# Kernel tuning notes

Hardware: AMD Instinct MI355X
Metric: run time of the kernel (lower is better)

Reference implementation:

```python
import jax, jax.numpy as jnp
import numpy as np

B, Fc, C, H, D, L = 128, 256, 256, 8, 32, 6  # batch, columns, dim, heads, head_dim, layers


def _ln(x, g, b, eps=1e-5):
    m = x.mean(-1, keepdims=True)
    v = ((x - m) ** 2).mean(-1, keepdims=True)
    return (x - m) * jax.lax.rsqrt(v + eps) * g + b


def setup_inputs() -> dict:
    key = jax.random.key(0)
    ks = jax.random.split(key, 16)
    s = 0.02  # weight init scale to keep 6-layer activations stable
    return {
        "x": jax.random.normal(ks[0], (B, Fc, C), jnp.float32),
        "col_emb": jax.random.normal(ks[1], (1, Fc, C), jnp.float32),
        "pos_emb": jax.random.normal(ks[2], (1, Fc + 1, C), jnp.float32),
        "col_bias": jax.random.normal(ks[3], (Fc, Fc), jnp.float32),
        "ln1_g": jnp.ones((L, C), jnp.float32),
        "ln1_b": jnp.zeros((L, C), jnp.float32),
        "qkv_w": jax.random.normal(ks[4], (L, C, 3 * C), jnp.float32) * s,
        "qkv_b": jnp.zeros((L, 3 * C), jnp.float32),
        "out_w": jax.random.normal(ks[5], (L, C, C), jnp.float32) * s,
        "out_b": jnp.zeros((L, C), jnp.float32),
        "ln2_g": jnp.ones((L, C), jnp.float32),
        "ln2_b": jnp.zeros((L, C), jnp.float32),
        "w1": jax.random.normal(ks[6], (L, C, 4 * C), jnp.float32) * s,
        "b1": jnp.zeros((L, 4 * C), jnp.float32),
        "w2": jax.random.normal(ks[7], (L, 4 * C, 2 * C), jnp.float32) * s,
        "b2": jnp.zeros((L, 2 * C), jnp.float32),
        "w3": jax.random.normal(ks[8], (L, C, C), jnp.float32) * s,
        "b3": jnp.zeros((L, C), jnp.float32),
        "fin_g": jnp.ones((C,), jnp.float32),
        "fin_b": jnp.zeros((C,), jnp.float32),
    }


def reference(x, col_emb, pos_emb, col_bias, ln1_g, ln1_b, qkv_w, qkv_b,
              out_w, out_b, ln2_g, ln2_b, w1, b1, w2, b2, w3, b3, fin_g, fin_b):
    Fdim = x.shape[1]
    h = x + col_emb[:, :Fdim] + pos_emb[:, 1:Fdim + 1]
    bias = col_bias[:Fdim, :Fdim]  # [T, T]
    scale = 1.0 / np.sqrt(D).astype(np.float32)
    params = (ln1_g, ln1_b, qkv_w, qkv_b, out_w, out_b, ln2_g, ln2_b,
              w1, b1, w2, b2, w3, b3)

    def block(xc, p):
        g1, be1, qw, qb, ow, ob, g2, be2, W1, B1, W2, B2, W3, B3 = p
        Bn, T, Cd = xc.shape
        hn = _ln(xc, g1, be1)
        qkv = hn @ qw + qb                              # [B,T,3C]
        q, k, v = jnp.split(qkv, 3, axis=-1)
        q = q.reshape(Bn, T, H, D)
        k = k.reshape(Bn, T, H, D)
        v = v.reshape(Bn, T, H, D)
        scores = jnp.einsum('bthd,bshd->bhts', q, k) * scale + bias[None, None]
        w = jax.nn.softmax(scores, axis=-1)             # dropout = identity (eval)
        attn = jnp.einsum('bhts,bshd->bthd', w, v).reshape(Bn, T, Cd)
        attn = attn @ ow + ob
        attn = attn + bias[None]                        # [1,T,T] broadcast, T==C
        xc = xc + attn
        hn2 = _ln(xc, g2, be2)
        u = jax.nn.gelu(hn2 @ W1 + B1, approximate=False)
        gl = u @ W2 + B2                                # [B,T,2C]
        a, gate = jnp.split(gl, 2, axis=-1)
        xc = xc + (a * jax.nn.sigmoid(gate)) @ W3 + B3
        return xc, None

    h, _ = jax.lax.scan(block, h, params)
    h = _ln(h, fin_g, fin_b)
    return h.mean(axis=1)  # pooling='mean' -> [B, C]
```

## Files before the change

kernel.cpp:

```cpp
#include <hip/hip_runtime.h>

typedef __bf16 bx8 __attribute__((ext_vector_type(8)));
typedef float fx4 __attribute__((ext_vector_type(4)));

#define GAS(p) ((const __attribute__((address_space(1))) void*)(const void*)(p))
#define LAS(p) ((__attribute__((address_space(3))) void*)(void*)(p))
#define WAITVM(n) do { asm volatile("s_waitcnt vmcnt(" #n ")" ::: "memory"); \
                       __builtin_amdgcn_sched_barrier(0); } while (0)
#define WAITLG0() do { asm volatile("s_waitcnt lgkmcnt(0)" ::: "memory"); \
                       __builtin_amdgcn_sched_barrier(0); } while (0)

__device__ __forceinline__ unsigned short f2bf(float f) {
  return __builtin_bit_cast(unsigned short, (__bf16)f);
}
__device__ __forceinline__ float bf2f(unsigned short s) {
  unsigned u = ((unsigned)s) << 16;
  return __builtin_bit_cast(float, u);
}

__global__ __launch_bounds__(256) void wtrans_kernel(const float* __restrict__ src,
                                                     unsigned short* __restrict__ dst,
                                                     int K, int N) {
  __shared__ unsigned short t[64][68];
  const int l = blockIdx.z;
  const float* s = src + (size_t)l * K * N;
  unsigned short* d = dst + (size_t)l * N * K;
  const int n0 = blockIdx.x * 64, k0 = blockIdx.y * 64;
  const int tx = threadIdx.x & 63, ty = threadIdx.x >> 6;
#pragma unroll
  for (int r = 0; r < 64; r += 4)
    t[tx][ty + r] = f2bf(s[(size_t)(k0 + ty + r) * N + n0 + tx]);
  __syncthreads();
#pragma unroll
  for (int r = 0; r < 64; r += 4)
    d[(size_t)(n0 + ty + r) * K + k0 + tx] = t[ty + r][tx];
}

__global__ __launch_bounds__(256) void embed_kernel(const float4* __restrict__ x,
                                                    const float4* __restrict__ ce,
                                                    const float4* __restrict__ pe,
                                                    float4* __restrict__ o) {
  int i = blockIdx.x * 256 + threadIdx.x;
  int c4 = i & 63;
  int t = (i >> 6) & 255;
  float4 a = x[i], b = ce[t * 64 + c4], p = pe[(t + 1) * 64 + c4];
  o[i] = make_float4(a.x + b.x + p.x, a.y + b.y + p.y, a.z + b.z + p.z, a.w + b.w + p.w);
}

template <int MODE>
__global__ __launch_bounds__(256) void ln_kernel(const float* __restrict__ x,
                                                 const float* __restrict__ gw,
                                                 const float* __restrict__ bw,
                                                 unsigned short* __restrict__ out,
                                                 float2* __restrict__ stats) {
  int row = blockIdx.x * 4 + (threadIdx.x >> 6);
  int lane = threadIdx.x & 63;
  const float4 v = *(const float4*)(x + (size_t)row * 256 + lane * 4);
  float s = v.x + v.y + v.z + v.w;
  float q = v.x * v.x + v.y * v.y + v.z * v.z + v.w * v.w;
#pragma unroll
  for (int off = 1; off < 64; off <<= 1) {
    s += __shfl_xor(s, off);
    q += __shfl_xor(q, off);
  }
  float mean = s * (1.0f / 256.0f);
  float rs = rsqrtf(q * (1.0f / 256.0f) - mean * mean + 1e-5f);
  if (MODE == 1) {
    if (lane == 0) stats[row] = make_float2(mean, rs);
    return;
  }
  float4 gv = *(const float4*)(gw + lane * 4);
  float4 bv = *(const float4*)(bw + lane * 4);
  ushort4 o;
  o.x = f2bf((v.x - mean) * rs * gv.x + bv.x);
  o.y = f2bf((v.y - mean) * rs * gv.y + bv.y);
  o.z = f2bf((v.z - mean) * rs * gv.z + bv.z);
  o.w = f2bf((v.w - mean) * rs * gv.w + bv.w);
  *(ushort4*)(out + (size_t)row * 256 + lane * 4) = o;
}

__global__ __launch_bounds__(256) void mean_part_kernel(const float* __restrict__ x,
                                                        const float2* __restrict__ stats,
                                                        float* __restrict__ part) {
  int b = blockIdx.x, half = blockIdx.y, c = threadIdx.x;
  const float* xb = x + (size_t)b * 65536 + half * 32768;
  const float2* st = stats + b * 256 + half * 128;
  float acc = 0.f;
#pragma unroll 4
  for (int t = 0; t < 128; ++t) {
    float2 s = st[t];
    acc += (xb[t * 256 + c] - s.x) * s.y;
  }
  part[(size_t)(b * 2 + half) * 256 + c] = acc;
}
__global__ __launch_bounds__(256) void mean_fin_kernel(const float* __restrict__ part,
                                                       const float* __restrict__ fg,
                                                       const float* __restrict__ fb,
                                                       float* __restrict__ out) {
  int b = blockIdx.x, c = threadIdx.x;
  out[b * 256 + c] =
      (part[(size_t)(2 * b) * 256 + c] + part[(size_t)(2 * b + 1) * 256 + c]) *
          (1.0f / 256.0f) * fg[c] + fb[c];
}

template <int EP>
__global__ __launch_bounds__(256) void gemm_kernel(const unsigned short* __restrict__ A,
                                                   const unsigned short* __restrict__ BT,
                                                   const float* __restrict__ bvec,
                                                   const float* __restrict__ cbias,
                                                   float* __restrict__ resid,
                                                   unsigned short* __restrict__ outb,
                                                   int N, int K) {
  __shared__ unsigned short lA[2][128 * 32];
  __shared__ unsigned short lB[2][128 * 32];
  const int tid = threadIdx.x;
  const int lane = tid & 63, w = tid >> 6;
  const int wr = w >> 1, wc = w & 1;
  const int g = lane >> 4, lr = lane & 15;
  const int m0 = blockIdx.y * 128, n0 = blockIdx.x * 128;
  fx4 acc[4][4] = {};

  auto STAGE = [&](int buf, int kk) {
#pragma unroll
    for (int r = 0; r < 2; ++r) {
      int u = r * 256 + tid;
      int row = u >> 2, sl = u & 3;
      int c = sl ^ ((row >> 1) & 3);
      __builtin_amdgcn_global_load_lds(GAS(A + (size_t)(m0 + row) * K + kk + c * 8),
                                       LAS(&lA[buf][u * 8]), 16, 0, 0);
      __builtin_amdgcn_global_load_lds(GAS(BT + (size_t)(n0 + row) * K + kk + c * 8),
                                       LAS(&lB[buf][u * 8]), 16, 0, 0);
    }
  };

  const int nt = K >> 5;
  STAGE(0, 0);
  STAGE(1, 32);
  for (int t = 0; t < nt; ++t) {
    if (t == nt - 1) WAITVM(0); else WAITVM(4);
    __builtin_amdgcn_s_barrier();
    const int buf = t & 1;
    bx8 af[4], bq[4];
#pragma unroll
    for (int i = 0; i < 4; ++i) {
      int row = wr * 64 + i * 16 + lr;
      af[i] = *(const bx8*)&lA[buf][row * 32 + (g ^ ((row >> 1) & 3)) * 8];
      int col = wc * 64 + i * 16 + lr;
      bq[i] = *(const bx8*)&lB[buf][col * 32 + (g ^ ((col >> 1) & 3)) * 8];
    }
    WAITLG0();
    __builtin_amdgcn_s_barrier();
    if (t + 2 < nt) STAGE(buf, (t + 2) * 32);
#pragma unroll
    for (int i = 0; i < 4; ++i)
#pragma unroll
      for (int j = 0; j < 4; ++j)
        acc[i][j] = __builtin_amdgcn_mfma_f32_16x16x32_bf16(bq[j], af[i], acc[i][j], 0, 0, 0);
  }

#pragma unroll
  for (int i = 0; i < 4; ++i) {
    const int m = m0 + wr * 64 + i * 16 + lr;
#pragma unroll
    for (int j = 0; j < 4; ++j) {
      const int nc = n0 + wc * 64 + j * 16 + g * 4;
      const float4 bv = *(const float4*)(bvec + nc);
      float v0 = acc[i][j][0] + bv.x, v1 = acc[i][j][1] + bv.y;
      float v2 = acc[i][j][2] + bv.z, v3 = acc[i][j][3] + bv.w;
      if constexpr (EP == 1) {
        v0 = 0.5f * v0 * (1.0f + erff(v0 * 0.70710678118654752f));
        v1 = 0.5f * v1 * (1.0f + erff(v1 * 0.70710678118654752f));
        v2 = 0.5f * v2 * (1.0f + erff(v2 * 0.70710678118654752f));
        v3 = 0.5f * v3 * (1.0f + erff(v3 * 0.70710678118654752f));
      }
      if constexpr (EP == 0 || EP == 1) {
        ushort4 st;
        st.x = f2bf(v0); st.y = f2bf(v1); st.z = f2bf(v2); st.w = f2bf(v3);
        *(ushort4*)(outb + (size_t)m * N + nc) = st;
      } else {
        if (nc < 512) {
          ushort4 st;
          st.x = f2bf(v0); st.y = f2bf(v1); st.z = f2bf(v2); st.w = f2bf(v3);
          *(ushort4*)(outb + (size_t)m * N + nc) = st;
        } else {
          unsigned short* vTp = (unsigned short*)resid;
          const int s = m & 255, b = m >> 8;
          const int hv = nc - 512;
          const int h = hv >> 5, d0 = hv & 31;
          const int jj = (s & 3) + 4 * ((s >> 4) & 1);
          const int ub = (s >> 5) * 128 + ((s >> 2) & 3) * 32 + d0;
          unsigned short* base = vTp + (size_t)(b * 8 + h) * 8192;
          const float vv[4] = {v0, v1, v2, v3};
#pragma unroll
          for (int r = 0; r < 4; ++r) {
            int u = ub + r;
            int up = (u & ~7) | ((u & 7) ^ ((u >> 3) & 7));
            base[up * 8 + jj] = f2bf(vv[r]);
          }
        }
      }
    }
  }
}

template <int EP>
__global__ __launch_bounds__(256) void gemm64_kernel(const unsigned short* __restrict__ A,
                                                     const unsigned short* __restrict__ BT,
                                                     const float* __restrict__ bvec,
                                                     const float* __restrict__ cbias,
                                                     float* __restrict__ resid,
                                                     int N, int K) {
  __shared__ unsigned short lA[2][64 * 32];
  __shared__ unsigned short lB[2][128 * 32];
  const int tid = threadIdx.x;
  const int lane = tid & 63, w = tid >> 6;
  const int g = lane >> 4, lr = lane & 15;
  const int m0 = blockIdx.y * 64, n0 = blockIdx.x * 128;
  fx4 acc[4][2] = {};

  auto STAGE = [&](int buf, int kk) {
    {
      int u = tid;
      int row = u >> 2, sl = u & 3;
      int c = sl ^ ((row >> 1) & 3);
      __builtin_amdgcn_global_load_lds(GAS(A + (size_t)(m0 + row) * K + kk + c * 8),
                                       LAS(&lA[buf][u * 8]), 16, 0, 0);
    }
#pragma unroll
    for (int r = 0; r < 2; ++r) {
      int u = r * 256 + tid;
      int row = u >> 2, sl = u & 3;
      int c = sl ^ ((row >> 1) & 3);
      __builtin_amdgcn_global_load_lds(GAS(BT + (size_t)(n0 + row) * K + kk + c * 8),
                                       LAS(&lB[buf][u * 8]), 16, 0, 0);
    }
  };

  const int nt = K >> 5;
  STAGE(0, 0);
  STAGE(1, 32);
  for (int t = 0; t < nt; ++t) {
    if (t == nt - 1) WAITVM(0); else WAITVM(3);
    __builtin_amdgcn_s_barrier();
    const int buf = t & 1;
    bx8 af[4], bq[2];
#pragma unroll
    for (int i = 0; i < 4; ++i) {
      int row = i * 16 + lr;
      af[i] = *(const bx8*)&lA[buf][row * 32 + (g ^ ((row >> 1) & 3)) * 8];
    }
#pragma unroll
    for (int j = 0; j < 2; ++j) {
      int col = w * 32 + j * 16 + lr;
      bq[j] = *(const bx8*)&lB[buf][col * 32 + (g ^ ((col >> 1) & 3)) * 8];
    }
    WAITLG0();
    __builtin_amdgcn_s_barrier();
    if (t + 2 < nt) STAGE(buf, (t + 2) * 32);
#pragma unroll
    for (int i = 0; i < 4; ++i)
#pragma unroll
      for (int j = 0; j < 2; ++j)
        acc[i][j] = __builtin_amdgcn_mfma_f32_16x16x32_bf16(bq[j], af[i], acc[i][j], 0, 0, 0);
  }

#pragma unroll
  for (int i = 0; i < 4; ++i) {
    const int m = m0 + i * 16 + lr;
#pragma unroll
    for (int j = 0; j < 2; ++j) {
      const int nc = n0 + w * 32 + j * 16 + g * 4;
      const float4 bv = *(const float4*)(bvec + nc);
      float v0 = acc[i][j][0] + bv.x, v1 = acc[i][j][1] + bv.y;
      float v2 = acc[i][j][2] + bv.z, v3 = acc[i][j][3] + bv.w;
      if constexpr (EP == 2) {
        const float4 cb = *(const float4*)(cbias + (size_t)(m & 255) * 256 + nc);
        v0 += cb.x; v1 += cb.y; v2 += cb.z; v3 += cb.w;
      }
      float4* rp = (float4*)(resid + (size_t)m * N + nc);
      float4 old = *rp;
      *rp = make_float4(old.x + v0, old.y + v1, old.z + v2, old.w + v3);
    }
  }
}

__global__ __launch_bounds__(256) void gemm_w2f64_kernel(const unsigned short* __restrict__ A,
                                                         const unsigned short* __restrict__ BT,
                                                         const float* __restrict__ b2,
                                                         unsigned short* __restrict__ gout) {
  __shared__ unsigned short lA[2][64 * 32];
  __shared__ unsigned short lBa[2][128 * 32];
  __shared__ unsigned short lBg[2][128 * 32];
  const int tid = threadIdx.x;
  const int lane = tid & 63, w = tid >> 6;
  const int g = lane >> 4, lr = lane & 15;
  const int m0 = blockIdx.y * 64, n0 = blockIdx.x * 128;
  fx4 aA[4][2] = {}, aG[4][2] = {};

  auto STAGE = [&](int buf, int kk) {
    {
      int u = tid;
      int row = u >> 2, sl = u & 3;
      int c = sl ^ ((row >> 1) & 3);
      __builtin_amdgcn_global_load_lds(GAS(A + (size_t)(m0 + row) * 1024 + kk + c * 8),
                                       LAS(&lA[buf][u * 8]), 16, 0, 0);
    }
#pragma unroll
    for (int r = 0; r < 2; ++r) {
      int u = r * 256 + tid;
      int row = u >> 2, sl = u & 3;
      int c = sl ^ ((row >> 1) & 3);
      __builtin_amdgcn_global_load_lds(GAS(BT + (size_t)(n0 + row) * 1024 + kk + c * 8),
                                       LAS(&lBa[buf][u * 8]), 16, 0, 0);
      __builtin_amdgcn_global_load_lds(GAS(BT + (size_t)(256 + n0 + row) * 1024 + kk + c * 8),
                                       LAS(&lBg[buf][u * 8]), 16, 0, 0);
    }
  };

  STAGE(0, 0);
  STAGE(1, 32);
  for (int t = 0; t < 32; ++t) {
    if (t == 31) WAITVM(0); else WAITVM(5);
    __builtin_amdgcn_s_barrier();
    const int buf = t & 1;
    bx8 af[4], ba[2], bg[2];
#pragma unroll
    for (int i = 0; i < 4; ++i) {
      int row = i * 16 + lr;
      af[i] = *(const bx8*)&lA[buf][row * 32 + (g ^ ((row >> 1) & 3)) * 8];
    }
#pragma unroll
    for (int j = 0; j < 2; ++j) {
      int col = w * 32 + j * 16 + lr;
      int sw = (g ^ ((col >> 1) & 3)) * 8;
      ba[j] = *(const bx8*)&lBa[buf][col * 32 + sw];
      bg[j] = *(const bx8*)&lBg[buf][col * 32 + sw];
    }
    WAITLG0();
    __builtin_amdgcn_s_barrier();
    if (t + 2 < 32) STAGE(buf, (t + 2) * 32);
#pragma unroll
    for (int i = 0; i < 4; ++i)
#pragma unroll
      for (int j = 0; j < 2; ++j) {
        aA[i][j] = __builtin_amdgcn_mfma_f32_16x16x32_bf16(ba[j], af[i], aA[i][j], 0, 0, 0);
        aG[i][j] = __builtin_amdgcn_mfma_f32_16x16x32_bf16(bg[j], af[i], aG[i][j], 0, 0, 0);
      }
  }

#pragma unroll
  for (int i = 0; i < 4; ++i) {
    const int m = m0 + i * 16 + lr;
#pragma unroll
    for (int j = 0; j < 2; ++j) {
      const int nc = n0 + w * 32 + j * 16 + g * 4;
      const float4 bva = *(const float4*)(b2 + nc);
      const float4 bvg = *(const float4*)(b2 + 256 + nc);
      float a0 = aA[i][j][0] + bva.x, a1 = aA[i][j][1] + bva.y;
      float a2 = aA[i][j][2] + bva.z, a3 = aA[i][j][3] + bva.w;
      float g0 = aG[i][j][0] + bvg.x, g1 = aG[i][j][1] + bvg.y;
      float g2 = aG[i][j][2] + bvg.z, g3 = aG[i][j][3] + bvg.w;
      ushort4 st;
      st.x = f2bf(a0 / (1.0f + __expf(-g0)));
      st.y = f2bf(a1 / (1.0f + __expf(-g1)));
      st.z = f2bf(a2 / (1.0f + __expf(-g2)));
      st.w = f2bf(a3 / (1.0f + __expf(-g3)));
      *(ushort4*)(gout + (size_t)m * 256 + nc) = st;
    }
  }
}

__global__ __launch_bounds__(256) void attn_kernel(const unsigned short* __restrict__ qkv,
                                                   const unsigned short* __restrict__ vT,
                                                   const float* __restrict__ cbias,
                                                   unsigned short* __restrict__ attnb) {
  __shared__ unsigned short Kl[256 * 32];
  __shared__ unsigned short Vl[1024 * 8];
  const int bh = blockIdx.x, b = bh >> 3, h = bh & 7;
  const int tid = threadIdx.x, lane = tid & 63, w = tid >> 6;
  const int g = lane >> 4, lr = lane & 15;
  const unsigned short* qb_ = qkv + (size_t)b * 196608;
  const unsigned short* vTb = vT + (size_t)bh * 8192;
#pragma unroll
  for (int r = 0; r < 4; ++r) {
    int u = r * 256 + tid;
    int s = u >> 2, sl = u & 3;
    int c = sl ^ ((s >> 1) & 3);
    __builtin_amdgcn_global_load_lds(GAS(qb_ + (size_t)s * 768 + 256 + h * 32 + c * 8),
                                     LAS(&Kl[u * 8]), 16, 0, 0);
    __builtin_amdgcn_global_load_lds(GAS(vTb + u * 8), LAS(&Vl[u * 8]), 16, 0, 0);
  }
  asm volatile("s_waitcnt vmcnt(0)" ::: "memory");
  __syncthreads();
  const float scale = 0.17677669529663689f;
  const fx4 zero = {0.f, 0.f, 0.f, 0.f};
#pragma unroll 1
  for (int it = 0; it < 4; ++it) {
    const int t = it * 64 + w * 16 + lr;
    bx8 qf = *(const bx8*)(qb_ + (size_t)t * 768 + h * 32 + g * 8);
    float p[16][4];
    float mx = -1e30f;
#pragma unroll
    for (int n = 0; n < 16; ++n) {
      int sr = n * 16 + lr;
      bx8 kf = *(const bx8*)&Kl[sr * 32 + (g ^ ((sr >> 1) & 3)) * 8];
      fx4 sc = __builtin_amdgcn_mfma_f32_16x16x32_bf16(kf, qf, zero, 0, 0, 0);
      const float4 cb = *(const float4*)(cbias + (size_t)t * 256 + n * 16 + g * 4);
      p[n][0] = sc[0] * scale + cb.x;
      p[n][1] = sc[1] * scale + cb.y;
      p[n][2] = sc[2] * scale + cb.z;
      p[n][3] = sc[3] * scale + cb.w;
      mx = fmaxf(mx, fmaxf(fmaxf(p[n][0], p[n][1]), fmaxf(p[n][2], p[n][3])));
    }
    mx = fmaxf(mx, __shfl_xor(mx, 16));
    mx = fmaxf(mx, __shfl_xor(mx, 32));
    float sum = 0.f;
    bx8 bq[8];
#pragma unroll
    for (int c = 0; c < 8; ++c) {
      union { bx8 v; unsigned short u[8]; } pk;
#pragma unroll
      for (int jj = 0; jj < 8; ++jj) {
        float e = __expf(p[2 * c + (jj >> 2)][jj & 3] - mx);
        sum += e;
        pk.u[jj] = f2bf(e);
      }
      bq[c] = pk.v;
    }
    sum += __shfl_xor(sum, 16);
    sum += __shfl_xor(sum, 32);
    const float inv = 1.0f / sum;
    fx4 oa0 = zero, oa1 = zero;
#pragma unroll
    for (int c = 0; c < 8; ++c) {
      int u0 = c * 128 + g * 32 + lr;
      int u0p = (u0 & ~7) | ((u0 & 7) ^ ((u0 >> 3) & 7));
      bx8 vf0 = *(const bx8*)&Vl[u0p * 8];
      oa0 = __builtin_amdgcn_mfma_f32_16x16x32_bf16(vf0, bq[c], oa0, 0, 0, 0);
      int u1 = u0 + 16;
      int u1p = (u1 & ~7) | ((u1 & 7) ^ ((u1 >> 3) & 7));
      bx8 vf1 = *(const bx8*)&Vl[u1p * 8];
      oa1 = __builtin_amdgcn_mfma_f32_16x16x32_bf16(vf1, bq[c], oa1, 0, 0, 0);
    }
    ushort4 o0, o1;
    o0.x = f2bf(oa0[0] * inv); o0.y = f2bf(oa0[1] * inv);
    o0.z = f2bf(oa0[2] * inv); o0.w = f2bf(oa0[3] * inv);
    o1.x = f2bf(oa1[0] * inv); o1.y = f2bf(oa1[1] * inv);
    o1.z = f2bf(oa1[2] * inv); o1.w = f2bf(oa1[3] * inv);
    unsigned short* orow = attnb + (size_t)(b * 256 + t) * 256 + h * 32;
    *(ushort4*)(orow + 4 * g) = o0;
    *(ushort4*)(orow + 16 + 4 * g) = o1;
  }
}

extern "C" void kernel_launch(void* const* d_in, const int* in_sizes, int n_in,
                              void* d_out, int out_size, void* d_ws, size_t ws_size,
                              hipStream_t stream) {
  (void)in_sizes; (void)n_in; (void)out_size; (void)ws_size;
  const float* x     = (const float*)d_in[0];
  const float* cemb  = (const float*)d_in[1];
  const float* pemb  = (const float*)d_in[2];
  const float* cbias = (const float*)d_in[3];
  const float* ln1g  = (const float*)d_in[4];
  const float* ln1b  = (const float*)d_in[5];
  const float* qkvw  = (const float*)d_in[6];
  const float* qkvb  = (const float*)d_in[7];
  const float* outw  = (const float*)d_in[8];
  const float* outbv = (const float*)d_in[9];
  const float* ln2g  = (const float*)d_in[10];
  const float* ln2b  = (const float*)d_in[11];
  const float* w1    = (const float*)d_in[12];
  const float* b1    = (const float*)d_in[13];
  const float* w2    = (const float*)d_in[14];
  const float* b2    = (const float*)d_in[15];
  const float* w3    = (const float*)d_in[16];
  const float* b3    = (const float*)d_in[17];
  const float* fing  = (const float*)d_in[18];
  const float* finb  = (const float*)d_in[19];

  char* ws = (char*)d_ws;
  float* x_res = (float*)(ws);
  unsigned short* hn   = (unsigned short*)(ws + 33554432);
  unsigned short* big  = (unsigned short*)(ws + 50331648);
  unsigned short* vT   = (unsigned short*)(ws + 100663296);
  unsigned short* wT   = (unsigned short*)(ws + 117440512);
  float2* stats = (float2*)(ws + 130809856);
  float* part  = (float*)big;

  unsigned short* qkvwT = wT;
  unsigned short* outwT = wT + 1179648;
  unsigned short* w1T   = wT + 1572864;
  unsigned short* w2T   = wT + 3145728;
  unsigned short* w3T   = wT + 6291456;

  wtrans_kernel<<<dim3(12, 4, 6), 256, 0, stream>>>(qkvw, qkvwT, 256, 768);
  wtrans_kernel<<<dim3(4, 4, 6), 256, 0, stream>>>(outw, outwT, 256, 256);
  wtrans_kernel<<<dim3(16, 4, 6), 256, 0, stream>>>(w1, w1T, 256, 1024);
  wtrans_kernel<<<dim3(8, 16, 6), 256, 0, stream>>>(w2, w2T, 1024, 512);
  wtrans_kernel<<<dim3(4, 4, 6), 256, 0, stream>>>(w3, w3T, 256, 256);
  embed_kernel<<<8192, 256, 0, stream>>>((const float4*)x, (const float4*)cemb,
                                         (const float4*)pemb, (float4*)x_res);
  for (int l = 0; l < 6; ++l) {
    ln_kernel<0><<<8192, 256, 0, stream>>>(x_res, ln1g + l * 256, ln1b + l * 256, hn, nullptr);
    gemm_kernel<4><<<dim3(6, 256), 256, 0, stream>>>(hn, qkvwT + (size_t)l * 196608,
                                                     qkvb + l * 768, nullptr, (float*)vT,
                                                     big, 768, 256);
    attn_kernel<<<1024, 256, 0, stream>>>(big, vT, cbias, hn);
    gemm64_kernel<2><<<dim3(2, 512), 256, 0, stream>>>(hn, outwT + (size_t)l * 65536,
                                                       outbv + l * 256, cbias, x_res,
                                                       256, 256);
    ln_kernel<0><<<8192, 256, 0, stream>>>(x_res, ln2g + l * 256, ln2b + l * 256, hn, nullptr);
    gemm_kernel<1><<<dim3(8, 256), 256, 0, stream>>>(hn, w1T + (size_t)l * 262144,
                                                     b1 + l * 1024, nullptr, nullptr, big,
                                                     1024, 256);
    gemm_w2f64_kernel<<<dim3(2, 512), 256, 0, stream>>>(big, w2T + (size_t)l * 524288,
                                                        b2 + l * 512, hn);
    gemm64_kernel<3><<<dim3(2, 512), 256, 0, stream>>>(hn, w3T + (size_t)l * 65536,
                                                       b3 + l * 256, nullptr, x_res,
                                                       256, 256);
  }
  ln_kernel<1><<<8192, 256, 0, stream>>>(x_res, nullptr, nullptr, nullptr, stats);
  mean_part_kernel<<<dim3(128, 2), 256, 0, stream>>>(x_res, stats, part);
  mean_fin_kernel<<<128, 256, 0, stream>>>(part, fing, finb, (float*)d_out);
}
```

Measured before the change: 1.540 ms.

## Fuse LayerNorm into residual GEMM epilogues and embedding, widen GEMM tiles

Removes the standalone LayerNorm launches by computing row statistics inside the out-proj and W3 GEMM epilogues, which now cover full 256-wide rows per block, and by fusing the first LN into the embedding kernel. The final-layer W3 GEMM writes mean/rstd stats for pooling directly. The gated W2 GEMM moves to 128x128 tiles, and attention hoists its Q fragment loads ahead of the K/V wait. This cuts 13 full-tensor read/write passes and launches, at the cost of fewer blocks for the fused GEMMs (512) and more registers and LDS per block.

```diff
diff --git a/kernel.cpp b/kernel.cpp
--- a/kernel.cpp
+++ b/kernel.cpp
@@ -36,26 +36,20 @@
     d[(size_t)(n0 + ty + r) * K + k0 + tx] = t[ty + r][tx];
 }
 
-__global__ __launch_bounds__(256) void embed_kernel(const float4* __restrict__ x,
-                                                    const float4* __restrict__ ce,
-                                                    const float4* __restrict__ pe,
-                                                    float4* __restrict__ o) {
-  int i = blockIdx.x * 256 + threadIdx.x;
-  int c4 = i & 63;
-  int t = (i >> 6) & 255;
-  float4 a = x[i], b = ce[t * 64 + c4], p = pe[(t + 1) * 64 + c4];
-  o[i] = make_float4(a.x + b.x + p.x, a.y + b.y + p.y, a.z + b.z + p.z, a.w + b.w + p.w);
-}
-
-template <int MODE>
-__global__ __launch_bounds__(256) void ln_kernel(const float* __restrict__ x,
-                                                 const float* __restrict__ gw,
-                                                 const float* __restrict__ bw,
-                                                 unsigned short* __restrict__ out,
-                                                 float2* __restrict__ stats) {
-  int row = blockIdx.x * 4 + (threadIdx.x >> 6);
-  int lane = threadIdx.x & 63;
-  const float4 v = *(const float4*)(x + (size_t)row * 256 + lane * 4);
+__global__ __launch_bounds__(256) void embed_ln_kernel(const float4* __restrict__ x,
+                                                       const float4* __restrict__ ce,
+                                                       const float4* __restrict__ pe,
+                                                       const float* __restrict__ gw,
+                                                       const float* __restrict__ bw,
+                                                       float4* __restrict__ xres,
+                                                       unsigned short* __restrict__ hn) {
+  const int row = blockIdx.x * 4 + (threadIdx.x >> 6);
+  const int lane = threadIdx.x & 63;
+  const int t = row & 255;
+  const size_t idx = (size_t)row * 64 + lane;
+  float4 a = x[idx], b = ce[t * 64 + lane], p = pe[(t + 1) * 64 + lane];
+  float4 v = make_float4(a.x + b.x + p.x, a.y + b.y + p.y, a.z + b.z + p.z, a.w + b.w + p.w);
+  xres[idx] = v;
   float s = v.x + v.y + v.z + v.w;
   float q = v.x * v.x + v.y * v.y + v.z * v.z + v.w * v.w;
 #pragma unroll
@@ -65,10 +59,6 @@
   }
   float mean = s * (1.0f / 256.0f);
   float rs = rsqrtf(q * (1.0f / 256.0f) - mean * mean + 1e-5f);
-  if (MODE == 1) {
-    if (lane == 0) stats[row] = make_float2(mean, rs);
-    return;
-  }
   float4 gv = *(const float4*)(gw + lane * 4);
   float4 bv = *(const float4*)(bw + lane * 4);
   ushort4 o;
@@ -76,7 +66,7 @@
   o.y = f2bf((v.y - mean) * rs * gv.y + bv.y);
   o.z = f2bf((v.z - mean) * rs * gv.z + bv.z);
   o.w = f2bf((v.w - mean) * rs * gv.w + bv.w);
-  *(ushort4*)(out + (size_t)row * 256 + lane * 4) = o;
+  *(ushort4*)(hn + (size_t)row * 256 + lane * 4) = o;
 }
 
 __global__ __launch_bounds__(256) void mean_part_kernel(const float* __restrict__ x,
@@ -107,7 +97,6 @@
 __global__ __launch_bounds__(256) void gemm_kernel(const unsigned short* __restrict__ A,
                                                    const unsigned short* __restrict__ BT,
                                                    const float* __restrict__ bvec,
-                                                   const float* __restrict__ cbias,
                                                    float* __restrict__ resid,
                                                    unsigned short* __restrict__ outb,
                                                    int N, int K) {
@@ -173,7 +162,7 @@
         v2 = 0.5f * v2 * (1.0f + erff(v2 * 0.70710678118654752f));
         v3 = 0.5f * v3 * (1.0f + erff(v3 * 0.70710678118654752f));
       }
-      if constexpr (EP == 0 || EP == 1) {
+      if constexpr (EP == 1) {
         ushort4 st;
         st.x = f2bf(v0); st.y = f2bf(v1); st.z = f2bf(v2); st.w = f2bf(v3);
         *(ushort4*)(outb + (size_t)m * N + nc) = st;
@@ -203,20 +192,25 @@
   }
 }
 
-template <int EP>
-__global__ __launch_bounds__(256) void gemm64_kernel(const unsigned short* __restrict__ A,
-                                                     const unsigned short* __restrict__ BT,
-                                                     const float* __restrict__ bvec,
-                                                     const float* __restrict__ cbias,
-                                                     float* __restrict__ resid,
-                                                     int N, int K) {
+template <int EP, int LNM>
+__global__ __launch_bounds__(256) void gemm_ln_kernel(const unsigned short* __restrict__ A,
+                                                      const unsigned short* __restrict__ BT,
+                                                      const float* __restrict__ bvec,
+                                                      const float* __restrict__ cbias,
+                                                      float* __restrict__ resid,
+                                                      const float* __restrict__ lnw,
+                                                      const float* __restrict__ lnb,
+                                                      unsigned short* __restrict__ hn,
+                                                      float2* __restrict__ stats,
+                                                      int K) {
   __shared__ unsigned short lA[2][64 * 32];
-  __shared__ unsigned short lB[2][128 * 32];
+  __shared__ unsigned short lB[2][256 * 32];
+  __shared__ float2 red[4][64];
   const int tid = threadIdx.x;
   const int lane = tid & 63, w = tid >> 6;
   const int g = lane >> 4, lr = lane & 15;
-  const int m0 = blockIdx.y * 64, n0 = blockIdx.x * 128;
-  fx4 acc[4][2] = {};
+  const int m0 = blockIdx.x * 64;
+  fx4 acc[4][4] = {};
 
   auto STAGE = [&](int buf, int kk) {
     {
@@ -227,11 +221,11 @@
                                        LAS(&lA[buf][u * 8]), 16, 0, 0);
     }
 #pragma unroll
-    for (int r = 0; r < 2; ++r) {
+    for (int r = 0; r < 4; ++r) {
       int u = r * 256 + tid;
       int row = u >> 2, sl = u & 3;
       int c = sl ^ ((row >> 1) & 3);
-      __builtin_amdgcn_global_load_lds(GAS(BT + (size_t)(n0 + row) * K + kk + c * 8),
+      __builtin_amdgcn_global_load_lds(GAS(BT + (size_t)row * K + kk + c * 8),
                                        LAS(&lB[buf][u * 8]), 16, 0, 0);
     }
   };
@@ -240,18 +234,18 @@
   STAGE(0, 0);
   STAGE(1, 32);
   for (int t = 0; t < nt; ++t) {
-    if (t == nt - 1) WAITVM(0); else WAITVM(3);
+    if (t == nt - 1) WAITVM(0); else WAITVM(5);
     __builtin_amdgcn_s_barrier();
     const int buf = t & 1;
-    bx8 af[4], bq[2];
+    bx8 af[4], bq[4];
 #pragma unroll
     for (int i = 0; i < 4; ++i) {
       int row = i * 16 + lr;
       af[i] = *(const bx8*)&lA[buf][row * 32 + (g ^ ((row >> 1) & 3)) * 8];
     }
 #pragma unroll
-    for (int j = 0; j < 2; ++j) {
-      int col = w * 32 + j * 16 + lr;
+    for (int j = 0; j < 4; ++j) {
+      int col = w * 64 + j * 16 + lr;
       bq[j] = *(const bx8*)&lB[buf][col * 32 + (g ^ ((col >> 1) & 3)) * 8];
     }
     WAITLG0();
@@ -260,16 +254,17 @@
 #pragma unroll
     for (int i = 0; i < 4; ++i)
 #pragma unroll
-      for (int j = 0; j < 2; ++j)
+      for (int j = 0; j < 4; ++j)
         acc[i][j] = __builtin_amdgcn_mfma_f32_16x16x32_bf16(bq[j], af[i], acc[i][j], 0, 0, 0);
   }
 
+  float s[4] = {0.f, 0.f, 0.f, 0.f}, q[4] = {0.f, 0.f, 0.f, 0.f};
 #pragma unroll
   for (int i = 0; i < 4; ++i) {
     const int m = m0 + i * 16 + lr;
 #pragma unroll
-    for (int j = 0; j < 2; ++j) {
-      const int nc = n0 + w * 32 + j * 16 + g * 4;
+    for (int j = 0; j < 4; ++j) {
+      const int nc = w * 64 + j * 16 + g * 4;
       const float4 bv = *(const float4*)(bvec + nc);
       float v0 = acc[i][j][0] + bv.x, v1 = acc[i][j][1] + bv.y;
       float v2 = acc[i][j][2] + bv.z, v3 = acc[i][j][3] + bv.w;
@@ -277,39 +272,82 @@
         const float4 cb = *(const float4*)(cbias + (size_t)(m & 255) * 256 + nc);
         v0 += cb.x; v1 += cb.y; v2 += cb.z; v3 += cb.w;
       }
-      float4* rp = (float4*)(resid + (size_t)m * N + nc);
+      float4* rp = (float4*)(resid + (size_t)m * 256 + nc);
       float4 old = *rp;
-      *rp = make_float4(old.x + v0, old.y + v1, old.z + v2, old.w + v3);
-    }
-  }
-}
-
-__global__ __launch_bounds__(256) void gemm_w2f64_kernel(const unsigned short* __restrict__ A,
-                                                         const unsigned short* __restrict__ BT,
-                                                         const float* __restrict__ b2,
-                                                         unsigned short* __restrict__ gout) {
-  __shared__ unsigned short lA[2][64 * 32];
+      v0 += old.x; v1 += old.y; v2 += old.z; v3 += old.w;
+      *rp = make_float4(v0, v1, v2, v3);
+      acc[i][j][0] = v0; acc[i][j][1] = v1; acc[i][j][2] = v2; acc[i][j][3] = v3;
+      s[i] += v0 + v1 + v2 + v3;
+      q[i] += v0 * v0 + v1 * v1 + v2 * v2 + v3 * v3;
+    }
+  }
+#pragma unroll
+  for (int i = 0; i < 4; ++i) {
+    s[i] += __shfl_xor(s[i], 16); s[i] += __shfl_xor(s[i], 32);
+    q[i] += __shfl_xor(q[i], 16); q[i] += __shfl_xor(q[i], 32);
+  }
+  if (lane < 16) {
+#pragma unroll
+    for (int i = 0; i < 4; ++i) red[w][i * 16 + lr] = make_float2(s[i], q[i]);
+  }
+  __syncthreads();
+  float mean[4], rs[4];
+#pragma unroll
+  for (int i = 0; i < 4; ++i) {
+    float2 r0 = red[0][i * 16 + lr], r1 = red[1][i * 16 + lr];
+    float2 r2 = red[2][i * 16 + lr], r3 = red[3][i * 16 + lr];
+    float S = r0.x + r1.x + r2.x + r3.x;
+    float Q = r0.y + r1.y + r2.y + r3.y;
+    mean[i] = S * (1.0f / 256.0f);
+    rs[i] = rsqrtf(Q * (1.0f / 256.0f) - mean[i] * mean[i] + 1e-5f);
+  }
+  if constexpr (LNM == 1) {
+    if (w == 0 && g == 0) {
+#pragma unroll
+      for (int i = 0; i < 4; ++i) stats[m0 + i * 16 + lr] = make_float2(mean[i], rs[i]);
+    }
+  } else {
+#pragma unroll
+    for (int i = 0; i < 4; ++i) {
+      const int m = m0 + i * 16 + lr;
+#pragma unroll
+      for (int j = 0; j < 4; ++j) {
+        const int nc = w * 64 + j * 16 + g * 4;
+        const float4 gv = *(const float4*)(lnw + nc);
+        const float4 bv2 = *(const float4*)(lnb + nc);
+        ushort4 st;
+        st.x = f2bf((acc[i][j][0] - mean[i]) * rs[i] * gv.x + bv2.x);
+        st.y = f2bf((acc[i][j][1] - mean[i]) * rs[i] * gv.y + bv2.y);
+        st.z = f2bf((acc[i][j][2] - mean[i]) * rs[i] * gv.z + bv2.z);
+        st.w = f2bf((acc[i][j][3] - mean[i]) * rs[i] * gv.w + bv2.w);
+        *(ushort4*)(hn + (size_t)m * 256 + nc) = st;
+      }
+    }
+  }
+}
+
+__global__ __launch_bounds__(256) void gemm_w2f_kernel(const unsigned short* __restrict__ A,
+                                                       const unsigned short* __restrict__ BT,
+                                                       const float* __restrict__ b2,
+                                                       unsigned short* __restrict__ gout) {
+  __shared__ unsigned short lA[2][128 * 32];
   __shared__ unsigned short lBa[2][128 * 32];
   __shared__ unsigned short lBg[2][128 * 32];
   const int tid = threadIdx.x;
   const int lane = tid & 63, w = tid >> 6;
+  const int wr = w >> 1, wc = w & 1;
   const int g = lane >> 4, lr = lane & 15;
-  const int m0 = blockIdx.y * 64, n0 = blockIdx.x * 128;
-  fx4 aA[4][2] = {}, aG[4][2] = {};
+  const int m0 = blockIdx.y * 128, n0 = blockIdx.x * 128;
+  fx4 aA[4][4] = {}, aG[4][4] = {};
 
   auto STAGE = [&](int buf, int kk) {
-    {
-      int u = tid;
+#pragma unroll
+    for (int r = 0; r < 2; ++r) {
+      int u = r * 256 + tid;
       int row = u >> 2, sl = u & 3;
       int c = sl ^ ((row >> 1) & 3);
       __builtin_amdgcn_global_load_lds(GAS(A + (size_t)(m0 + row) * 1024 + kk + c * 8),
                                        LAS(&lA[buf][u * 8]), 16, 0, 0);
-    }
-#pragma unroll
-    for (int r = 0; r < 2; ++r) {
-      int u = r * 256 + tid;
-      int row = u >> 2, sl = u & 3;
-      int c = sl ^ ((row >> 1) & 3);
       __builtin_amdgcn_global_load_lds(GAS(BT + (size_t)(n0 + row) * 1024 + kk + c * 8),
                                        LAS(&lBa[buf][u * 8]), 16, 0, 0);
       __builtin_amdgcn_global_load_lds(GAS(BT + (size_t)(256 + n0 + row) * 1024 + kk + c * 8),
@@ -320,21 +358,18 @@
   STAGE(0, 0);
   STAGE(1, 32);
   for (int t = 0; t < 32; ++t) {
-    if (t == 31) WAITVM(0); else WAITVM(5);
+    if (t == 31) WAITVM(0); else WAITVM(6);
     __builtin_amdgcn_s_barrier();
     const int buf = t & 1;
-    bx8 af[4], ba[2], bg[2];
+    bx8 af[4], ba[4], bg[4];
 #pragma unroll
     for (int i = 0; i < 4; ++i) {
-      int row = i * 16 + lr;
+      int row = wr * 64 + i * 16 + lr;
       af[i] = *(const bx8*)&lA[buf][row * 32 + (g ^ ((row >> 1) & 3)) * 8];
-    }
-#pragma unroll
-    for (int j = 0; j < 2; ++j) {
-      int col = w * 32 + j * 16 + lr;
+      int col = wc * 64 + i * 16 + lr;
       int sw = (g ^ ((col >> 1) & 3)) * 8;
-      ba[j] = *(const bx8*)&lBa[buf][col * 32 + sw];
-      bg[j] = *(const bx8*)&lBg[buf][col * 32 + sw];
+      ba[i] = *(const bx8*)&lBa[buf][col * 32 + sw];
+      bg[i] = *(const bx8*)&lBg[buf][col * 32 + sw];
     }
     WAITLG0();
     __builtin_amdgcn_s_barrier();
@@ -342,7 +377,7 @@
 #pragma unroll
     for (int i = 0; i < 4; ++i)
 #pragma unroll
-      for (int j = 0; j < 2; ++j) {
+      for (int j = 0; j < 4; ++j) {
         aA[i][j] = __builtin_amdgcn_mfma_f32_16x16x32_bf16(ba[j], af[i], aA[i][j], 0, 0, 0);
         aG[i][j] = __builtin_amdgcn_mfma_f32_16x16x32_bf16(bg[j], af[i], aG[i][j], 0, 0, 0);
       }
@@ -350,10 +385,10 @@
 
 #pragma unroll
   for (int i = 0; i < 4; ++i) {
-    const int m = m0 + i * 16 + lr;
-#pragma unroll
-    for (int j = 0; j < 2; ++j) {
-      const int nc = n0 + w * 32 + j * 16 + g * 4;
+    const int m = m0 + wr * 64 + i * 16 + lr;
+#pragma unroll
+    for (int j = 0; j < 4; ++j) {
+      const int nc = n0 + wc * 64 + j * 16 + g * 4;
       const float4 bva = *(const float4*)(b2 + nc);
       const float4 bvg = *(const float4*)(b2 + 256 + nc);
       float a0 = aA[i][j][0] + bva.x, a1 = aA[i][j][1] + bva.y;
@@ -390,6 +425,10 @@
                                      LAS(&Kl[u * 8]), 16, 0, 0);
     __builtin_amdgcn_global_load_lds(GAS(vTb + u * 8), LAS(&Vl[u * 8]), 16, 0, 0);
   }
+  bx8 qf[4];
+#pragma unroll
+  for (int it = 0; it < 4; ++it)
+    qf[it] = *(const bx8*)(qb_ + (size_t)(it * 64 + w * 16 + lr) * 768 + h * 32 + g * 8);
   asm volatile("s_waitcnt vmcnt(0)" ::: "memory");
   __syncthreads();
   const float scale = 0.17677669529663689f;
@@ -397,14 +436,13 @@
 #pragma unroll 1
   for (int it = 0; it < 4; ++it) {
     const int t = it * 64 + w * 16 + lr;
-    bx8 qf = *(const bx8*)(qb_ + (size_t)t * 768 + h * 32 + g * 8);
     float p[16][4];
     float mx = -1e30f;
 #pragma unroll
     for (int n = 0; n < 16; ++n) {
       int sr = n * 16 + lr;
       bx8 kf = *(const bx8*)&Kl[sr * 32 + (g ^ ((sr >> 1) & 3)) * 8];
-      fx4 sc = __builtin_amdgcn_mfma_f32_16x16x32_bf16(kf, qf, zero, 0, 0, 0);
+      fx4 sc = __builtin_amdgcn_mfma_f32_16x16x32_bf16(kf, qf[it], zero, 0, 0, 0);
       const float4 cb = *(const float4*)(cbias + (size_t)t * 256 + n * 16 + g * 4);
       p[n][0] = sc[0] * scale + cb.x;
       p[n][1] = sc[1] * scale + cb.y;
@@ -498,28 +536,36 @@
   wtrans_kernel<<<dim3(16, 4, 6), 256, 0, stream>>>(w1, w1T, 256, 1024);
   wtrans_kernel<<<dim3(8, 16, 6), 256, 0, stream>>>(w2, w2T, 1024, 512);
   wtrans_kernel<<<dim3(4, 4, 6), 256, 0, stream>>>(w3, w3T, 256, 256);
-  embed_kernel<<<8192, 256, 0, stream>>>((const float4*)x, (const float4*)cemb,
-                                         (const float4*)pemb, (float4*)x_res);
+  embed_ln_kernel<<<8192, 256, 0, stream>>>((const float4*)x, (const float4*)cemb,
+                                            (const float4*)pemb, ln1g, ln1b,
+                                            (float4*)x_res, hn);
   for (int l = 0; l < 6; ++l) {
-    ln_kernel<0><<<8192, 256, 0, stream>>>(x_res, ln1g + l * 256, ln1b + l * 256, hn, nullptr);
     gemm_kernel<4><<<dim3(6, 256), 256, 0, stream>>>(hn, qkvwT + (size_t)l * 196608,
-                                                     qkvb + l * 768, nullptr, (float*)vT,
-                                                     big, 768, 256);
+                                                     qkvb + l * 768, (float*)vT, big,
+                                                     768, 256);
     attn_kernel<<<1024, 256, 0, stream>>>(big, vT, cbias, hn);
-    gemm64_kernel<2><<<dim3(2, 512), 256, 0, stream>>>(hn, outwT + (size_t)l * 65536,
-                                                       outbv + l * 256, cbias, x_res,
-                                                       256, 256);
-    ln_kernel<0><<<8192, 256, 0, stream>>>(x_res, ln2g + l * 256, ln2b + l * 256, hn, nullptr);
+    gemm_ln_kernel<2, 0><<<512, 256, 0, stream>>>(hn, outwT + (size_t)l * 65536,
+                                                  outbv + l * 256, cbias, x_res,
+                                                  ln2g + l * 256, ln2b + l * 256, hn,
+                                                  nullptr, 256);
     gemm_kernel<1><<<dim3(8, 256), 256, 0, stream>>>(hn, w1T + (size_t)l * 262144,
-                                                     b1 + l * 1024, nullptr, nullptr, big,
+                                                     b1 + l * 1024, nullptr, big,
                                                      1024, 256);
-    gemm_w2f64_kernel<<<dim3(2, 512), 256, 0, stream>>>(big, w2T + (size_t)l * 524288,
-                                                        b2 + l * 512, hn);
-    gemm64_kernel<3><<<dim3(2, 512), 256, 0, stream>>>(hn, w3T + (size_t)l * 65536,
-                                                       b3 + l * 256, nullptr, x_res,
-                                                       256, 256);
-  }
-  ln_kernel<1><<<8192, 256, 0, stream>>>(x_res, nullptr, nullptr, nullptr, stats);
+    gemm_w2f_kernel<<<dim3(2, 256), 256, 0, stream>>>(big, w2T + (size_t)l * 524288,
+                                                      b2 + l * 512, hn);
+    if (l < 5) {
+      gemm_ln_kernel<3, 0><<<512, 256, 0, stream>>>(hn, w3T + (size_t)l * 65536,
+                                                    b3 + l * 256, nullptr, x_res,
+                                                    ln1g + (l + 1) * 256,
+                                                    ln1b + (l + 1) * 256, hn,
+                                                    nullptr, 256);
+    } else {
+      gemm_ln_kernel<3, 1><<<512, 256, 0, stream>>>(hn, w3T + (size_t)l * 65536,
+                                                    b3 + l * 256, nullptr, x_res,
+                                                    nullptr, nullptr, nullptr,
+                                                    stats, 256);
+    }
+  }
   mean_part_kernel<<<dim3(128, 2), 256, 0, stream>>>(x_res, stats, part);
   mean_fin_kernel<<<128, 256, 0, stream>>>(part, fing, finb, (float*)d_out);
 }
```

New measurement: 1.611 ms. 4.6% more time.
